# Kernel optimization log

Hardware: AMD Instinct MI355X
Metric: run time of the kernel (lower is better)

The kernel has to match this reference:

```python
import jax, jax.numpy as jnp
import numpy as np

N = 2_000_000      # total nodes
D = 128            # in_channel
B = 1024           # batch_size (num graphs)
STEPS = 3          # processing_step
NUM_LAYER = 1


def setup_inputs() -> dict:
    key = jax.random.key(0)
    ks = jax.random.split(key, 6)
    x = jax.random.normal(ks[0], (N, D), dtype=jnp.float32)
    batch_index = jnp.sort(jax.random.randint(ks[1], (N,), 0, B, dtype=jnp.int64))
    s = 1.0 / np.sqrt(D)  # PyTorch LSTM init scale: U(-1/sqrt(hidden), 1/sqrt(hidden))
    W_ih = jax.random.uniform(ks[2], (4 * D, 2 * D), jnp.float32, -s, s)
    W_hh = jax.random.uniform(ks[3], (4 * D, D), jnp.float32, -s, s)
    b_ih = jax.random.uniform(ks[4], (4 * D,), jnp.float32, -s, s)
    b_hh = jax.random.uniform(ks[5], (4 * D,), jnp.float32, -s, s)
    return {"x": x, "batch_index": batch_index, "W_ih": W_ih, "W_hh": W_hh,
            "b_ih": b_ih, "b_hh": b_hh}


def _lstm_cell(inp, h, c, W_ih, W_hh, b_ih, b_hh):
    # PyTorch gate order: i, f, g, o
    gates = inp @ W_ih.T + b_ih + h @ W_hh.T + b_hh  # [B, 4D]
    i, f, g, o = jnp.split(gates, 4, axis=-1)
    c = jax.nn.sigmoid(f) * c + jax.nn.sigmoid(i) * jnp.tanh(g)
    h = jax.nn.sigmoid(o) * jnp.tanh(c)
    return h, c


def reference(x, batch_index, W_ih, W_hh, b_ih, b_hh):
    h = jnp.zeros((B, D), x.dtype)
    c = jnp.zeros((B, D), x.dtype)
    q_star = jnp.zeros((B, 2 * D), x.dtype)
    for _ in range(STEPS):
        h, c = _lstm_cell(q_star, h, c, W_ih, W_hh, b_ih, b_hh)
        q = h  # [B, D]
        # attention logits per node
        e = jnp.sum(x * q[batch_index], axis=-1, keepdims=True)  # [N, 1]
        # segment softmax over nodes of each graph
        m = jax.ops.segment_max(e, batch_index, num_segments=B)  # [B, 1]
        ee = jnp.exp(e - m[batch_index])
        ssum = jax.ops.segment_sum(ee, batch_index, num_segments=B)  # [B, 1]
        a = ee / (ssum[batch_index] + 1e-16)  # [N, 1]
        # weighted pooling per graph
        r = jax.ops.segment_sum(a * x, batch_index, num_segments=B)  # [B, D]
        q_star = jnp.concatenate([q, r], axis=-1)  # [B, 2D]
    return q_star
```

## Files before the change

kernel.cpp:

```cpp
#include <hip/hip_runtime.h>

#define NN 2000000
#define DD 128
#define BB 1024
#define STEPS 3

__global__ void prep_kernel(const float* __restrict__ W_ih,
                            const float* __restrict__ W_hh,
                            const float* __restrict__ b_ih,
                            const float* __restrict__ b_hh,
                            float* __restrict__ WT, float* __restrict__ bias) {
    int idx = blockIdx.x * blockDim.x + threadIdx.x;
    if (idx < 384 * 512) {
        int k = idx >> 9;
        int j = idx & 511;
        WT[idx] = (k < 256) ? W_ih[j * 256 + k] : W_hh[j * 128 + (k - 256)];
    }
    if (idx < 512) bias[idx] = b_ih[idx] + b_hh[idx];
}

__global__ void segstart_kernel(const int* __restrict__ bi, int* __restrict__ start) {
    int n = blockIdx.x * blockDim.x + threadIdx.x;
    if (n >= NN) return;
    int v = bi[n];
    int p = (n == 0) ? -1 : bi[n - 1];
    for (int t = p + 1; t <= v; ++t) start[t] = n;
    if (n == NN - 1) {
        for (int t = v + 1; t <= BB; ++t) start[t] = NN;
    }
}

__device__ __forceinline__ float sigmoid_f(float x) { return 1.0f / (1.0f + __expf(-x)); }
__device__ __forceinline__ float tanh_f(float x) {
    float e = __expf(2.0f * x);
    return 1.0f - 2.0f / (e + 1.0f);
}

__launch_bounds__(256)
__global__ void lstm_kernel(const float* __restrict__ q_star,
                            float* __restrict__ h, float* __restrict__ c,
                            const float* __restrict__ WT,
                            const float* __restrict__ bias) {
    __shared__ float in_lds[4][384];
    __shared__ float gate_lds[4][512];
    const int b0 = blockIdx.x * 4;
    const int tid = threadIdx.x;

    for (int idx = tid; idx < 4 * 384; idx += 256) {
        int bb = idx / 384;
        int k = idx - bb * 384;
        in_lds[bb][k] = (k < 256) ? q_star[(b0 + bb) * 256 + k]
                                  : h[(b0 + bb) * 128 + (k - 256)];
    }
    __syncthreads();

    const int j0 = tid, j1 = tid + 256;
    float acc[4][2] = {};
    for (int k = 0; k < 384; k += 4) {
        float4 a0 = *(const float4*)&in_lds[0][k];
        float4 a1 = *(const float4*)&in_lds[1][k];
        float4 a2 = *(const float4*)&in_lds[2][k];
        float4 a3 = *(const float4*)&in_lds[3][k];
        const float* f0 = (const float*)&a0;
        const float* f1 = (const float*)&a1;
        const float* f2 = (const float*)&a2;
        const float* f3 = (const float*)&a3;
#pragma unroll
        for (int kk = 0; kk < 4; ++kk) {
            float w0 = WT[(k + kk) * 512 + j0];
            float w1 = WT[(k + kk) * 512 + j1];
            acc[0][0] = fmaf(f0[kk], w0, acc[0][0]);
            acc[0][1] = fmaf(f0[kk], w1, acc[0][1]);
            acc[1][0] = fmaf(f1[kk], w0, acc[1][0]);
            acc[1][1] = fmaf(f1[kk], w1, acc[1][1]);
            acc[2][0] = fmaf(f2[kk], w0, acc[2][0]);
            acc[2][1] = fmaf(f2[kk], w1, acc[2][1]);
            acc[3][0] = fmaf(f3[kk], w0, acc[3][0]);
            acc[3][1] = fmaf(f3[kk], w1, acc[3][1]);
        }
    }
    float bj0 = bias[j0], bj1 = bias[j1];
#pragma unroll
    for (int bb = 0; bb < 4; ++bb) {
        gate_lds[bb][j0] = acc[bb][0] + bj0;
        gate_lds[bb][j1] = acc[bb][1] + bj1;
    }
    __syncthreads();

#pragma unroll
    for (int it = 0; it < 2; ++it) {
        int item = tid + it * 256;
        int bb = item >> 7;
        int d = item & 127;
        int b = b0 + bb;
        float gi = gate_lds[bb][d];
        float gf = gate_lds[bb][128 + d];
        float gg = gate_lds[bb][256 + d];
        float go = gate_lds[bb][384 + d];
        float cn = sigmoid_f(gf) * c[b * 128 + d] + sigmoid_f(gi) * tanh_f(gg);
        float hn = sigmoid_f(go) * tanh_f(cn);
        c[b * 128 + d] = cn;
        h[b * 128 + d] = hn;
    }
}

__launch_bounds__(256)
__global__ void att_kernel(const float* __restrict__ x,
                           const float* __restrict__ h,
                           const int* __restrict__ start,
                           float* __restrict__ q_star) {
    const int b = blockIdx.x;
    const int tid = threadIdx.x;
    const int wave = tid >> 6;
    const int lane = tid & 63;
    const int g = lane >> 4;
    const int sl = lane & 15;
    const int c0 = 4 * sl;

    const int s0 = start[b];
    const int s1 = start[b + 1];

    float4 qlo = *(const float4*)&h[b * 128 + c0];
    float4 qhi = *(const float4*)&h[b * 128 + 64 + c0];

    float mA = -1e30f, sA = 0.0f;
    float4 rAlo = make_float4(0.f, 0.f, 0.f, 0.f), rAhi = make_float4(0.f, 0.f, 0.f, 0.f);
    float mB = -1e30f, sB = 0.0f;
    float4 rBlo = make_float4(0.f, 0.f, 0.f, 0.f), rBhi = make_float4(0.f, 0.f, 0.f, 0.f);

    if (s0 < s1) {
        const int lastn = s1 - 1;
        const int nbase = s0 + (wave * 4 + g) * 2;

        int pA = min(nbase, lastn);
        int pB = min(nbase + 1, lastn);
        float4 xal = *(const float4*)&x[(size_t)pA * 128 + c0];
        float4 xah = *(const float4*)&x[(size_t)pA * 128 + 64 + c0];
        float4 xbl = *(const float4*)&x[(size_t)pB * 128 + c0];
        float4 xbh = *(const float4*)&x[(size_t)pB * 128 + 64 + c0];

        for (int n0 = nbase; n0 < s1; n0 += 32) {
            int qA = min(n0 + 32, lastn);
            int qB = min(n0 + 33, lastn);
            float4 nal = *(const float4*)&x[(size_t)qA * 128 + c0];
            float4 nah = *(const float4*)&x[(size_t)qA * 128 + 64 + c0];
            float4 nbl = *(const float4*)&x[(size_t)qB * 128 + c0];
            float4 nbh = *(const float4*)&x[(size_t)qB * 128 + 64 + c0];

            float dA = xal.x * qlo.x + xal.y * qlo.y + xal.z * qlo.z + xal.w * qlo.w
                     + xah.x * qhi.x + xah.y * qhi.y + xah.z * qhi.z + xah.w * qhi.w;
            float dB = xbl.x * qlo.x + xbl.y * qlo.y + xbl.z * qlo.z + xbl.w * qlo.w
                     + xbh.x * qhi.x + xbh.y * qhi.y + xbh.z * qhi.z + xbh.w * qhi.w;
#pragma unroll
            for (int off = 8; off >= 1; off >>= 1) {
                dA += __shfl_xor(dA, off, 64);
                dB += __shfl_xor(dB, off, 64);
            }

            {
                float nm = fmaxf(mA, dA);
                float fac = __expf(mA - nm);
                float w = __expf(dA - nm);
                sA = sA * fac + w;
                rAlo.x = rAlo.x * fac + w * xal.x;
                rAlo.y = rAlo.y * fac + w * xal.y;
                rAlo.z = rAlo.z * fac + w * xal.z;
                rAlo.w = rAlo.w * fac + w * xal.w;
                rAhi.x = rAhi.x * fac + w * xah.x;
                rAhi.y = rAhi.y * fac + w * xah.y;
                rAhi.z = rAhi.z * fac + w * xah.z;
                rAhi.w = rAhi.w * fac + w * xah.w;
                mA = nm;
            }
            {
                bool vB = (n0 + 1) < s1;
                float e = vB ? dB : -1e30f;
                float nm = fmaxf(mB, e);
                float fac = __expf(mB - nm);
                float w = vB ? __expf(e - nm) : 0.0f;
                sB = sB * fac + w;
                rBlo.x = rBlo.x * fac + w * xbl.x;
                rBlo.y = rBlo.y * fac + w * xbl.y;
                rBlo.z = rBlo.z * fac + w * xbl.z;
                rBlo.w = rBlo.w * fac + w * xbl.w;
                rBhi.x = rBhi.x * fac + w * xbh.x;
                rBhi.y = rBhi.y * fac + w * xbh.y;
                rBhi.z = rBhi.z * fac + w * xbh.z;
                rBhi.w = rBhi.w * fac + w * xbh.w;
                mB = nm;
            }

            xal = nal; xah = nah; xbl = nbl; xbh = nbh;
        }
    }

    float M = fmaxf(mA, mB);
    float eA = __expf(mA - M);
    float eB = __expf(mB - M);
    float S = sA * eA + sB * eB;
    float4 Rlo, Rhi;
    Rlo.x = rAlo.x * eA + rBlo.x * eB;
    Rlo.y = rAlo.y * eA + rBlo.y * eB;
    Rlo.z = rAlo.z * eA + rBlo.z * eB;
    Rlo.w = rAlo.w * eA + rBlo.w * eB;
    Rhi.x = rAhi.x * eA + rBhi.x * eB;
    Rhi.y = rAhi.y * eA + rBhi.y * eB;
    Rhi.z = rAhi.z * eA + rBhi.z * eB;
    Rhi.w = rAhi.w * eA + rBhi.w * eB;

    __shared__ float m_sh[16];
    __shared__ float s_sh[16];
    __shared__ float r_sh[16][128];

    const int slot = wave * 4 + g;
    *(float4*)&r_sh[slot][c0] = Rlo;
    *(float4*)&r_sh[slot][64 + c0] = Rhi;
    if (sl == 0) {
        m_sh[slot] = M;
        s_sh[slot] = S;
    }
    __syncthreads();

    if (tid < 128) {
        int d = tid;
        float Mf = -1e30f;
#pragma unroll
        for (int p = 0; p < 16; ++p) Mf = fmaxf(Mf, m_sh[p]);
        float Sf = 0.0f, Rf = 0.0f;
#pragma unroll
        for (int p = 0; p < 16; ++p) {
            float fac = __expf(m_sh[p] - Mf);
            Sf += s_sh[p] * fac;
            Rf += r_sh[p][d] * fac;
        }
        float rfin = Rf / (Sf + 1e-16f);
        q_star[b * 256 + d] = h[b * 128 + d];
        q_star[b * 256 + 128 + d] = rfin;
    }
}

extern "C" void kernel_launch(void* const* d_in, const int* in_sizes, int n_in,
                              void* d_out, int out_size, void* d_ws, size_t ws_size,
                              hipStream_t stream) {
    const float* x    = (const float*)d_in[0];
    const int*   bidx = (const int*)d_in[1];
    const float* W_ih = (const float*)d_in[2];
    const float* W_hh = (const float*)d_in[3];
    const float* b_ih = (const float*)d_in[4];
    const float* b_hh = (const float*)d_in[5];
    float* q_star = (float*)d_out;

    char* ws = (char*)d_ws;
    float* WT    = (float*)(ws);
    float* bias  = (float*)(ws + 786432);
    float* h     = (float*)(ws + 788480);
    float* c     = (float*)(ws + 1312768);
    int*   start = (int*)  (ws + 1837056);

    hipMemsetAsync(h, 0, BB * DD * sizeof(float), stream);
    hipMemsetAsync(c, 0, BB * DD * sizeof(float), stream);
    hipMemsetAsync(q_star, 0, BB * 2 * DD * sizeof(float), stream);

    prep_kernel<<<(384 * 512 + 255) / 256, 256, 0, stream>>>(W_ih, W_hh, b_ih, b_hh, WT, bias);
    segstart_kernel<<<(NN + 255) / 256, 256, 0, stream>>>(bidx, start);

    for (int step = 0; step < STEPS; ++step) {
        lstm_kernel<<<256, 256, 0, stream>>>(q_star, h, c, WT, bias);
        att_kernel<<<BB, 256, 0, stream>>>(x, h, start, q_star);
    }
}
```

Baseline: 1.719 ms.

## Split per-graph attention across eight blocks with a separate merge kernel

The single attention kernel, which used one block per graph, becomes a partial kernel launching eight blocks per graph. Each block runs an online softmax over one contiguous chunk of that graph's nodes and writes its max, sum and weighted row to a workspace buffer. A small merge kernel then combines the eight partials with log-sum-exp rescaling. The aim is more parallelism and memory-level concurrency for the x stream, which is about 1 GB per step. The cost is an extra launch, partial-buffer traffic, and halving per-thread loads in flight, since the two-node unroll is dropped.

Result: no change. 1.738 ms (+1.1%).

```diff
diff --git a/kernel.cpp b/kernel.cpp
--- a/kernel.cpp
+++ b/kernel.cpp
@@ -4,6 +4,8 @@
 #define DD 128
 #define BB 1024
 #define STEPS 3
+#define SPLIT 8
+#define PSTRIDE 132
 
 __global__ void prep_kernel(const float* __restrict__ W_ih,
                             const float* __restrict__ W_hh,
@@ -104,120 +106,78 @@
     }
 }
 
-__launch_bounds__(256)
-__global__ void att_kernel(const float* __restrict__ x,
-                           const float* __restrict__ h,
-                           const int* __restrict__ start,
-                           float* __restrict__ q_star) {
-    const int b = blockIdx.x;
+__launch_bounds__(256, 8)
+__global__ void att_partial_kernel(const float* __restrict__ x,
+                                   const float* __restrict__ h,
+                                   const int* __restrict__ start,
+                                   float* __restrict__ partials) {
+    const int b = blockIdx.x >> 3;
+    const int sp = blockIdx.x & (SPLIT - 1);
     const int tid = threadIdx.x;
-    const int wave = tid >> 6;
-    const int lane = tid & 63;
-    const int g = lane >> 4;
-    const int sl = lane & 15;
+    const int g16 = tid >> 4;
+    const int sl = tid & 15;
     const int c0 = 4 * sl;
 
     const int s0 = start[b];
     const int s1 = start[b + 1];
+    const int len = s1 - s0;
+    const int chunk = (len + SPLIT - 1) >> 3;
+    const int a0 = s0 + sp * chunk;
+    const int a1 = min(a0 + chunk, s1);
 
     float4 qlo = *(const float4*)&h[b * 128 + c0];
     float4 qhi = *(const float4*)&h[b * 128 + 64 + c0];
 
-    float mA = -1e30f, sA = 0.0f;
-    float4 rAlo = make_float4(0.f, 0.f, 0.f, 0.f), rAhi = make_float4(0.f, 0.f, 0.f, 0.f);
-    float mB = -1e30f, sB = 0.0f;
-    float4 rBlo = make_float4(0.f, 0.f, 0.f, 0.f), rBhi = make_float4(0.f, 0.f, 0.f, 0.f);
-
-    if (s0 < s1) {
-        const int lastn = s1 - 1;
-        const int nbase = s0 + (wave * 4 + g) * 2;
-
-        int pA = min(nbase, lastn);
-        int pB = min(nbase + 1, lastn);
-        float4 xal = *(const float4*)&x[(size_t)pA * 128 + c0];
-        float4 xah = *(const float4*)&x[(size_t)pA * 128 + 64 + c0];
-        float4 xbl = *(const float4*)&x[(size_t)pB * 128 + c0];
-        float4 xbh = *(const float4*)&x[(size_t)pB * 128 + 64 + c0];
-
-        for (int n0 = nbase; n0 < s1; n0 += 32) {
-            int qA = min(n0 + 32, lastn);
-            int qB = min(n0 + 33, lastn);
-            float4 nal = *(const float4*)&x[(size_t)qA * 128 + c0];
-            float4 nah = *(const float4*)&x[(size_t)qA * 128 + 64 + c0];
-            float4 nbl = *(const float4*)&x[(size_t)qB * 128 + c0];
-            float4 nbh = *(const float4*)&x[(size_t)qB * 128 + 64 + c0];
-
-            float dA = xal.x * qlo.x + xal.y * qlo.y + xal.z * qlo.z + xal.w * qlo.w
-                     + xah.x * qhi.x + xah.y * qhi.y + xah.z * qhi.z + xah.w * qhi.w;
-            float dB = xbl.x * qlo.x + xbl.y * qlo.y + xbl.z * qlo.z + xbl.w * qlo.w
-                     + xbh.x * qhi.x + xbh.y * qhi.y + xbh.z * qhi.z + xbh.w * qhi.w;
-#pragma unroll
-            for (int off = 8; off >= 1; off >>= 1) {
-                dA += __shfl_xor(dA, off, 64);
-                dB += __shfl_xor(dB, off, 64);
-            }
-
-            {
-                float nm = fmaxf(mA, dA);
-                float fac = __expf(mA - nm);
-                float w = __expf(dA - nm);
-                sA = sA * fac + w;
-                rAlo.x = rAlo.x * fac + w * xal.x;
-                rAlo.y = rAlo.y * fac + w * xal.y;
-                rAlo.z = rAlo.z * fac + w * xal.z;
-                rAlo.w = rAlo.w * fac + w * xal.w;
-                rAhi.x = rAhi.x * fac + w * xah.x;
-                rAhi.y = rAhi.y * fac + w * xah.y;
-                rAhi.z = rAhi.z * fac + w * xah.z;
-                rAhi.w = rAhi.w * fac + w * xah.w;
-                mA = nm;
-            }
-            {
-                bool vB = (n0 + 1) < s1;
-                float e = vB ? dB : -1e30f;
-                float nm = fmaxf(mB, e);
-                float fac = __expf(mB - nm);
-                float w = vB ? __expf(e - nm) : 0.0f;
-                sB = sB * fac + w;
-                rBlo.x = rBlo.x * fac + w * xbl.x;
-                rBlo.y = rBlo.y * fac + w * xbl.y;
-                rBlo.z = rBlo.z * fac + w * xbl.z;
-                rBlo.w = rBlo.w * fac + w * xbl.w;
-                rBhi.x = rBhi.x * fac + w * xbh.x;
-                rBhi.y = rBhi.y * fac + w * xbh.y;
-                rBhi.z = rBhi.z * fac + w * xbh.z;
-                rBhi.w = rBhi.w * fac + w * xbh.w;
-                mB = nm;
-            }
-
-            xal = nal; xah = nah; xbl = nbl; xbh = nbh;
+    float m = -1e30f, s = 0.0f;
+    float4 rlo = make_float4(0.f, 0.f, 0.f, 0.f);
+    float4 rhi = make_float4(0.f, 0.f, 0.f, 0.f);
+
+    if (a0 < a1) {
+        const int lastn = a1 - 1;
+        const int n0 = a0 + g16;
+
+        int cur = min(n0, lastn);
+        float4 xl = *(const float4*)&x[(size_t)cur * 128 + c0];
+        float4 xh = *(const float4*)&x[(size_t)cur * 128 + 64 + c0];
+
+        for (int n = n0; n < a1; n += 16) {
+            int nxt = min(n + 16, lastn);
+            float4 nl = *(const float4*)&x[(size_t)nxt * 128 + c0];
+            float4 nh = *(const float4*)&x[(size_t)nxt * 128 + 64 + c0];
+
+            float d = xl.x * qlo.x + xl.y * qlo.y + xl.z * qlo.z + xl.w * qlo.w
+                    + xh.x * qhi.x + xh.y * qhi.y + xh.z * qhi.z + xh.w * qhi.w;
+#pragma unroll
+            for (int off = 8; off >= 1; off >>= 1)
+                d += __shfl_xor(d, off, 64);
+
+            float nm = fmaxf(m, d);
+            float fac = __expf(m - nm);
+            float w = __expf(d - nm);
+            s = s * fac + w;
+            rlo.x = rlo.x * fac + w * xl.x;
+            rlo.y = rlo.y * fac + w * xl.y;
+            rlo.z = rlo.z * fac + w * xl.z;
+            rlo.w = rlo.w * fac + w * xl.w;
+            rhi.x = rhi.x * fac + w * xh.x;
+            rhi.y = rhi.y * fac + w * xh.y;
+            rhi.z = rhi.z * fac + w * xh.z;
+            rhi.w = rhi.w * fac + w * xh.w;
+            m = nm;
+
+            xl = nl; xh = nh;
         }
     }
-
-    float M = fmaxf(mA, mB);
-    float eA = __expf(mA - M);
-    float eB = __expf(mB - M);
-    float S = sA * eA + sB * eB;
-    float4 Rlo, Rhi;
-    Rlo.x = rAlo.x * eA + rBlo.x * eB;
-    Rlo.y = rAlo.y * eA + rBlo.y * eB;
-    Rlo.z = rAlo.z * eA + rBlo.z * eB;
-    Rlo.w = rAlo.w * eA + rBlo.w * eB;
-    Rhi.x = rAhi.x * eA + rBhi.x * eB;
-    Rhi.y = rAhi.y * eA + rBhi.y * eB;
-    Rhi.z = rAhi.z * eA + rBhi.z * eB;
-    Rhi.w = rAhi.w * eA + rBhi.w * eB;
 
     __shared__ float m_sh[16];
     __shared__ float s_sh[16];
     __shared__ float r_sh[16][128];
 
-    const int slot = wave * 4 + g;
-    *(float4*)&r_sh[slot][c0] = Rlo;
-    *(float4*)&r_sh[slot][64 + c0] = Rhi;
+    *(float4*)&r_sh[g16][c0] = rlo;
+    *(float4*)&r_sh[g16][64 + c0] = rhi;
     if (sl == 0) {
-        m_sh[slot] = M;
-        s_sh[slot] = S;
+        m_sh[g16] = m;
+        s_sh[g16] = s;
     }
     __syncthreads();
 
@@ -233,10 +193,31 @@
             Sf += s_sh[p] * fac;
             Rf += r_sh[p][d] * fac;
         }
-        float rfin = Rf / (Sf + 1e-16f);
-        q_star[b * 256 + d] = h[b * 128 + d];
-        q_star[b * 256 + 128 + d] = rfin;
-    }
+        float* P = &partials[(size_t)(b * SPLIT + sp) * PSTRIDE];
+        if (d == 0) { P[0] = Mf; P[1] = Sf; }
+        P[4 + d] = Rf;
+    }
+}
+
+__launch_bounds__(128)
+__global__ void att_merge_kernel(const float* __restrict__ partials,
+                                 const float* __restrict__ h,
+                                 float* __restrict__ q_star) {
+    const int b = blockIdx.x;
+    const int d = threadIdx.x;
+    const float* P = &partials[(size_t)b * SPLIT * PSTRIDE];
+    float M = -1e30f;
+#pragma unroll
+    for (int p = 0; p < SPLIT; ++p) M = fmaxf(M, P[p * PSTRIDE]);
+    float S = 0.0f, R = 0.0f;
+#pragma unroll
+    for (int p = 0; p < SPLIT; ++p) {
+        float fac = __expf(P[p * PSTRIDE] - M);
+        S += P[p * PSTRIDE + 1] * fac;
+        R += P[p * PSTRIDE + 4 + d] * fac;
+    }
+    q_star[b * 256 + d] = h[b * 128 + d];
+    q_star[b * 256 + 128 + d] = R / (S + 1e-16f);
 }
 
 extern "C" void kernel_launch(void* const* d_in, const int* in_sizes, int n_in,
@@ -251,11 +232,12 @@
     float* q_star = (float*)d_out;
 
     char* ws = (char*)d_ws;
-    float* WT    = (float*)(ws);
-    float* bias  = (float*)(ws + 786432);
-    float* h     = (float*)(ws + 788480);
-    float* c     = (float*)(ws + 1312768);
-    int*   start = (int*)  (ws + 1837056);
+    float* WT       = (float*)(ws);
+    float* bias     = (float*)(ws + 786432);
+    float* h        = (float*)(ws + 788480);
+    float* c        = (float*)(ws + 1312768);
+    int*   start    = (int*)  (ws + 1837056);
+    float* partials = (float*)(ws + 1841408);
 
     hipMemsetAsync(h, 0, BB * DD * sizeof(float), stream);
     hipMemsetAsync(c, 0, BB * DD * sizeof(float), stream);
@@ -266,6 +248,7 @@
 
     for (int step = 0; step < STEPS; ++step) {
         lstm_kernel<<<256, 256, 0, stream>>>(q_star, h, c, WT, bias);
-        att_kernel<<<BB, 256, 0, stream>>>(x, h, start, q_star);
-    }
-}
+        att_partial_kernel<<<BB * SPLIT, 256, 0, stream>>>(x, h, start, partials);
+        att_merge_kernel<<<BB, 128, 0, stream>>>(partials, h, q_star);
+    }
+}
```
